# Optimization experiments

Hardware: AMD Instinct MI355X
Metric: run time of the kernel (lower is better)

The kernel has to match this reference:

```python
import jax, jax.numpy as jnp
import numpy as np

GRID_SIZE = 8
SPLINE_ORDER = 3
GRID_LO, GRID_HI = -1.0, 1.0
EPS = 1e-5  # InstanceNorm2d default eps
C = 16
K = GRID_SIZE + SPLINE_ORDER  # number of B-spline basis channels per input channel


def make_grid():
    h = (GRID_HI - GRID_LO) / GRID_SIZE
    # extended knot vector, length grid_size + 2*spline_order + 1
    return jnp.arange(-SPLINE_ORDER, GRID_SIZE + SPLINE_ORDER + 1, dtype=jnp.float32) * h + GRID_LO


def bspline_bases(x, grid):
    # x: [B,C,H,W] -> bases: [B,C,H,W,K] via Cox-de Boor recursion
    xu = x[..., None]
    bases = ((xu >= grid[:-1]) & (xu < grid[1:])).astype(x.dtype)
    for k in range(1, SPLINE_ORDER + 1):
        left = grid[:-(k + 1)]
        right = grid[k:-1]
        delta = jnp.where(right == left, jnp.ones_like(right), right - left)
        bases = ((xu - left) / delta) * bases[..., :-1] + \
                ((grid[k + 1:] - xu) / (grid[k + 1:] - grid[1:-k])) * bases[..., 1:]
    return bases


def conv2d(x, w):
    # NCHW conv, stride 1, padding 1 (kernel 3x3), bias=False as in KANConv2DLayer
    return jax.lax.conv_general_dilated(
        x, w, window_strides=(1, 1), padding=[(1, 1), (1, 1)],
        dimension_numbers=('NCHW', 'OIHW', 'NCHW'))


def instance_norm(x):
    # nn.InstanceNorm2d(affine=False): normalize over H,W per (N,C)
    m = jnp.mean(x, axis=(2, 3), keepdims=True)
    v = jnp.var(x, axis=(2, 3), keepdims=True)
    return (x - m) * jax.lax.rsqrt(v + EPS)


def prelu(x, a):
    return jnp.where(x >= 0, x, a * x)


def kan_conv_layer(x, base_w, spline_w, prelu_a, grid):
    base_out = conv2d(jax.nn.silu(x), base_w)
    b = bspline_bases(x, grid)                      # [B,C,H,W,K]
    B, Cx, H, W, Kx = b.shape
    b = jnp.moveaxis(b, -1, 2).reshape(B, Cx * Kx, H, W)
    spline_out = conv2d(b, spline_w)
    return prelu(instance_norm(base_out + spline_out), prelu_a)


def setup_inputs() -> dict:
    key = jax.random.key(0)
    ks = jax.random.split(key, 5)
    s = 0.05
    return {
        'x': jax.random.normal(ks[0], (4, C, 512, 512), jnp.float32),
        'base_w1': jax.random.normal(ks[1], (C, C, 3, 3), jnp.float32) * s,
        'spline_w1': jax.random.normal(ks[2], (C, C * K, 3, 3), jnp.float32) * s,
        'prelu_a1': jnp.float32(0.25),
        'base_w2': jax.random.normal(ks[3], (C, C, 3, 3), jnp.float32) * s,
        'spline_w2': jax.random.normal(ks[4], (C, C * K, 3, 3), jnp.float32) * s,
        'prelu_a2': jnp.float32(0.25),
    }


def reference(x, base_w1, spline_w1, prelu_a1, base_w2, spline_w2, prelu_a2):
    grid = make_grid()
    y = kan_conv_layer(x, base_w1, spline_w1, prelu_a1, grid)
    y = kan_conv_layer(y, base_w2, spline_w2, prelu_a2, grid)
    return jax.nn.sigmoid(y)
```

## Files before the change

kernel.cpp:

```cpp
#include <hip/hip_runtime.h>
#include <cstddef>
#include <cstdint>

#define HW    512
#define CCH   16
#define HTILE 18
#define NPIX  324
#define NSLOT 12

typedef _Float16 f16x8 __attribute__((ext_vector_type(8)));
typedef float    f32x4 __attribute__((ext_vector_type(4)));

__device__ __forceinline__ float h2f(ushort u) {
    _Float16 h = __builtin_bit_cast(_Float16, u);
    return (float)h;
}
__device__ __forceinline__ ushort f2h(float f) {
    _Float16 h = (_Float16)f;
    return __builtin_bit_cast(ushort, h);
}
__device__ __forceinline__ uint pack2h(float a, float b) {
    return (uint)f2h(a) | ((uint)f2h(b) << 16);
}

__device__ __forceinline__ void derived12(float x, uint* u) {
    float si = x / (1.0f + __expf(-x));
    float t  = fmaf(x, 4.0f, 7.0f);
    t = fminf(fmaxf(t, -1.0f), 15.0f);
    float ft = floorf(t);
    int   ci = (int)ft;
    float uu = t - ft;
    float um = 1.0f - uu;
    float u2 = uu * uu, m2 = um * um;
    float u3 = u2 * uu, m3 = m2 * um;
    const float c16 = 0.16666667f, c23 = 0.66666667f;
    float w0 = u3 * c16;
    float w3 = m3 * c16;
    float w2 = fmaf(0.5f, u3, c23 - u2);
    float w1 = fmaf(0.5f, m3, c23 - m2);
    uint64_t P = (uint64_t)f2h(w3)
               | ((uint64_t)f2h(w2) << 16)
               | ((uint64_t)f2h(w1) << 32)
               | ((uint64_t)f2h(w0) << 48);
    int s = 16 * ci - 48;
    int d = s >> 6;
    int e = s & 63;
    uint64_t Q = P << e;
    uint64_t R = (P >> (63 - e)) >> 1;
    uint64_t O0 = (d == 0) ? Q : (d == -1) ? R : 0ull;
    uint64_t O1 = (d == 1) ? Q : (d ==  0) ? R : 0ull;
    uint64_t O2 = (d == 2) ? Q : (d ==  1) ? R : 0ull;
    O2 = (O2 & 0x0000ffffffffffffull) | ((uint64_t)f2h(si) << 48);
    u[0] = (uint)O0; u[1] = (uint)(O0 >> 32);
    u[2] = (uint)O1; u[3] = (uint)(O1 >> 32);
    u[4] = (uint)O2; u[5] = (uint)(O2 >> 32);
}

__global__ void __launch_bounds__(64) prep_w(
    const float* __restrict__ bw1, const float* __restrict__ sw1,
    const float* __restrict__ bw2, const float* __restrict__ sw2,
    uint4* __restrict__ wtab1, uint4* __restrict__ wtab2,
    float* __restrict__ part1, float* __restrict__ part2)
{
    const int s    = blockIdx.x;
    const int lane = threadIdx.x;
    const float* bw; const float* sw; uint4* wt;
    if (blockIdx.y == 0) { bw = bw1; sw = sw1; wt = wtab1; }
    else                 { bw = bw2; sw = sw2; wt = wtab2; }

    if (s == 0) {
        float* p = (blockIdx.y == 0) ? part1 : part2;
        p[lane] = 0.0f;
        p[64 + lane] = 0.0f;
    }

    const int co = lane & 15, q = lane >> 4;
    const int chunk = s / 27, sl = s - chunk * 27;
    uint u[4];
#pragma unroll
    for (int jj = 0; jj < 4; ++jj) {
        float w[2];
#pragma unroll
        for (int h = 0; h < 2; ++h) {
            int j   = jj * 2 + h;
            int kl  = 32 * sl + 8 * q + j;
            int tap = kl / 96;
            int r   = kl - tap * 96;
            int ci  = r / 12;
            int kv  = r - ci * 12;
            int cin = chunk * 8 + ci;
            w[h] = (kv == 11) ? bw[(co * 16 + cin) * 9 + tap]
                              : sw[(co * 176 + cin * 11 + kv) * 9 + tap];
        }
        u[jj] = pack2h(w[0], w[1]);
    }
    wt[s * 64 + lane] = make_uint4(u[0], u[1], u[2], u[3]);
}

template<bool IN_H, bool OUT_H, bool NORM_IN>
__global__ __launch_bounds__(256, 2) void conv_mfma(
    const void* __restrict__ in_v,
    const uint4* __restrict__ wtab,
    void* __restrict__ out_v,
    const float* __restrict__ stats_in,
    const float* __restrict__ a_in,
    float* __restrict__ part_out)
{
    __shared__ uint4 dt16[NSLOT * NPIX];
    __shared__ float sn[32];

    const int tid  = threadIdx.x;
    const int lane = tid & 63;
    const int wv   = tid >> 6;
    const int m    = lane & 15;
    const int q    = lane >> 4;
    const int bx0  = blockIdx.x * 16;
    const int by0  = blockIdx.y * 16;
    const int b    = blockIdx.z;

    const float*  inf = (const float*)in_v;
    const ushort* inh = (const ushort*)in_v;

    float pa = 0.0f;
    if (NORM_IN) {
        pa = *a_in;
        if (tid < 32) sn[tid] = stats_in[b * 32 + tid];
    }

    f32x4 acc[4];
#pragma unroll
    for (int t = 0; t < 4; ++t) acc[t] = f32x4{0.f, 0.f, 0.f, 0.f};

#pragma unroll 1
    for (int chunk = 0; chunk < 2; ++chunk) {
        __syncthreads();

        float v0[6], v1[6];
        uint  bofs[6], cps[6];
        bool  live[6];
#pragma unroll
        for (int k = 0; k < 6; ++k) {
            int it  = tid + k * 256;
            bool lv = (it < NPIX * 4);
            int cp  = it / NPIX;
            int pix = it - cp * NPIX;
            int py  = pix / 18;
            int px  = pix - py * 18;
            int gy  = by0 + py - 1;
            int gx  = bx0 + px - 1;
            bool ok = lv && ((unsigned)gy < (unsigned)HW)
                         && ((unsigned)gx < (unsigned)HW);
            live[k] = lv;
            cps[k]  = (uint)cp;
            bofs[k] = (uint)(cp * 3 * NPIX + pix);
            float a = -1.0e9f, c = -1.0e9f;
            if (ok) {
                size_t base = ((size_t)(b * CCH + chunk * 8 + cp * 2) << 18)
                            + ((size_t)gy << 9) + gx;
                if (IN_H) { a = h2f(inh[base]); c = h2f(inh[base + (1u << 18)]); }
                else      { a = inf[base];      c = inf[base + (1u << 18)]; }
            }
            v0[k] = a; v1[k] = c;
        }

        uint4 wf[27];
#pragma unroll
        for (int s = 0; s < 27; ++s) wf[s] = wtab[(chunk * 27 + s) * 64 + lane];

#pragma unroll
        for (int k = 0; k < 6; ++k) {
            if (live[k]) {
                float a0 = v0[k], c0 = v1[k];
                if (NORM_IN) {
                    int ci2 = (chunk * 8 + (int)cps[k] * 2) * 2;
                    a0 = (a0 - sn[ci2])     * sn[ci2 + 1];
                    a0 = (a0 >= 0.f) ? a0 : pa * a0;
                    c0 = (c0 - sn[ci2 + 2]) * sn[ci2 + 3];
                    c0 = (c0 >= 0.f) ? c0 : pa * c0;
                }
                uint uA[6], uB[6];
                derived12(a0, uA);
                derived12(c0, uB);
                uint bo = bofs[k];
                dt16[bo]            = make_uint4(uA[0], uA[1], uA[2], uA[3]);
                dt16[bo + NPIX]     = make_uint4(uA[4], uA[5], uB[0], uB[1]);
                dt16[bo + 2 * NPIX] = make_uint4(uB[2], uB[3], uB[4], uB[5]);
            }
        }
        __syncthreads();

        const uint pixbase = (uint)(wv * 72 + m);
#pragma unroll
        for (int j = 0; j < 3; ++j) {
            const uint slotoff = (uint)((j * 4 + q) * NPIX) + pixbase;
#pragma unroll
            for (int tdx = 0; tdx < 3; ++tdx) {
                f16x8 brow[6];
#pragma unroll
                for (int r6 = 0; r6 < 6; ++r6)
                    brow[r6] = *reinterpret_cast<const f16x8*>(
                        &dt16[slotoff + (uint)(r6 * HTILE + tdx)]);
#pragma unroll
                for (int tdy = 0; tdy < 3; ++tdy) {
                    const int s = (tdy * 3 + tdx) * 3 + j;
#pragma unroll
                    for (int t = 0; t < 4; ++t) {
                        acc[t] = __builtin_amdgcn_mfma_f32_16x16x32_f16(
                            __builtin_bit_cast(f16x8, wf[s]), brow[t + tdy],
                            acc[t], 0, 0, 0);
                    }
                }
            }
        }
    }

#pragma unroll
    for (int t = 0; t < 4; ++t) {
        int oy = by0 + wv * 4 + t;
#pragma unroll
        for (int r = 0; r < 4; ++r) {
            int co = q * 4 + r;
            size_t idx = ((size_t)(b * CCH + co) << 18) + ((size_t)oy << 9) + (bx0 + m);
            if (OUT_H) ((ushort*)out_v)[idx] = f2h(acc[t][r]);
            else       ((float*)out_v)[idx]  = acc[t][r];
        }
    }

    float s4[4], q4[4];
#pragma unroll
    for (int r = 0; r < 4; ++r) {
        s4[r] = acc[0][r] + acc[1][r] + acc[2][r] + acc[3][r];
        q4[r] = fmaf(acc[0][r], acc[0][r],
                fmaf(acc[1][r], acc[1][r],
                fmaf(acc[2][r], acc[2][r], acc[3][r] * acc[3][r])));
    }
#pragma unroll
    for (int off = 8; off > 0; off >>= 1) {
#pragma unroll
        for (int r = 0; r < 4; ++r) {
            s4[r] += __shfl_xor(s4[r], off);
            q4[r] += __shfl_xor(q4[r], off);
        }
    }
    __syncthreads();
    float* scr = (float*)dt16;
    if (m == 0) {
#pragma unroll
        for (int r = 0; r < 4; ++r) {
            scr[(wv * 16 + q * 4 + r) * 2 + 0] = s4[r];
            scr[(wv * 16 + q * 4 + r) * 2 + 1] = q4[r];
        }
    }
    __syncthreads();
    if (tid < 32) {
        int co = tid >> 1, which = tid & 1;
        float v = scr[(0 * 16 + co) * 2 + which] + scr[(1 * 16 + co) * 2 + which]
                + scr[(2 * 16 + co) * 2 + which] + scr[(3 * 16 + co) * 2 + which];
        atomicAdd(&part_out[(size_t)(b * CCH + co) * 2 + which], v);
    }
}

__global__ void __launch_bounds__(64) reduce_final(
    const float* __restrict__ part, float* __restrict__ stats)
{
    const int bc = threadIdx.x;
    const float inv = 1.0f / 262144.0f;
    float s  = part[bc * 2];
    float qq = part[bc * 2 + 1];
    float mval = s * inv;
    float var  = qq * inv - mval * mval;
    stats[bc * 2]     = mval;
    stats[bc * 2 + 1] = rsqrtf(var + 1e-5f);
}

__global__ void __launch_bounds__(256) final_sigmoid(
    float* __restrict__ out, const float* __restrict__ stats,
    const float* __restrict__ a_ptr)
{
    const float a = *a_ptr;
    const int i4 = blockIdx.x * 256 + threadIdx.x;
    const int bc = i4 >> 16;
    const float mm = stats[bc * 2];
    const float rr = stats[bc * 2 + 1];
    float4 v = reinterpret_cast<float4*>(out)[i4];
    float t;
    t = (v.x - mm) * rr; t = (t >= 0.f) ? t : a * t; v.x = 1.0f / (1.0f + __expf(-t));
    t = (v.y - mm) * rr; t = (t >= 0.f) ? t : a * t; v.y = 1.0f / (1.0f + __expf(-t));
    t = (v.z - mm) * rr; t = (t >= 0.f) ? t : a * t; v.z = 1.0f / (1.0f + __expf(-t));
    t = (v.w - mm) * rr; t = (t >= 0.f) ? t : a * t; v.w = 1.0f / (1.0f + __expf(-t));
    reinterpret_cast<float4*>(out)[i4] = v;
}

extern "C" void kernel_launch(void* const* d_in, const int* in_sizes, int n_in,
                              void* d_out, int out_size, void* d_ws, size_t ws_size,
                              hipStream_t stream)
{
    const float* x        = (const float*)d_in[0];
    const float* base_w1  = (const float*)d_in[1];
    const float* spline_w1= (const float*)d_in[2];
    const float* prelu_a1 = (const float*)d_in[3];
    const float* base_w2  = (const float*)d_in[4];
    const float* spline_w2= (const float*)d_in[5];
    const float* prelu_a2 = (const float*)d_in[6];
    float* out_f = (float*)d_out;
    char*  wsb   = (char*)d_ws;

    ushort* z1h    = (ushort*)wsb;
    uint4*  wtab1  = (uint4*)(wsb + 33554432);
    uint4*  wtab2  = (uint4*)(wsb + 33609728);
    float*  part1  = (float*)(wsb + 33665024);
    float*  part2  = (float*)(wsb + 33665536);
    float*  stats1 = (float*)(wsb + 33666048);
    float*  stats2 = (float*)(wsb + 33666560);

    dim3 cgrid(HW / 16, HW / 16, 4);
    dim3 cblk(256);

    prep_w<<<dim3(54, 2), 64, 0, stream>>>(base_w1, spline_w1, base_w2, spline_w2,
                                           wtab1, wtab2, part1, part2);

    conv_mfma<false, true, false><<<cgrid, cblk, 0, stream>>>(
        x, wtab1, z1h, nullptr, nullptr, part1);
    reduce_final<<<1, 64, 0, stream>>>(part1, stats1);

    conv_mfma<true, false, true><<<cgrid, cblk, 0, stream>>>(
        z1h, wtab2, out_f, stats1, prelu_a1, part2);
    reduce_final<<<1, 64, 0, stream>>>(part2, stats2);

    final_sigmoid<<<16384, cblk, 0, stream>>>(out_f, stats2, prelu_a2);
}
```

Before: 356.0 us.

## Shrink conv tile to 12 rows, raise occupancy, prefetch next chunk loads

Cuts the output tile from 16x16 to 16x12 rows, which shrinks the LDS staging buffer so three blocks can fit per CU (launch bounds raised to 3). The global loads for the second channel chunk are issued before the first chunk's MFMA loop, so their latency overlaps with compute. Pixel-to-thread mapping is rewritten so each thread loads four channels per pixel. In exchange, halo overhead per output rises (14 staged rows for 12 outputs instead of 18 for 16), the last row of blocks is partial and needs guards, and register pressure under the tighter launch bound may cause spills.

```diff
diff --git a/kernel.cpp b/kernel.cpp
--- a/kernel.cpp
+++ b/kernel.cpp
@@ -4,8 +4,10 @@
 
 #define HW    512
 #define CCH   16
+#define TR    12
 #define HTILE 18
-#define NPIX  324
+#define HTR   14
+#define NPIX2 252
 #define NSLOT 12
 
 typedef _Float16 f16x8 __attribute__((ext_vector_type(8)));
@@ -98,7 +100,7 @@
 }
 
 template<bool IN_H, bool OUT_H, bool NORM_IN>
-__global__ __launch_bounds__(256, 2) void conv_mfma(
+__global__ __launch_bounds__(256, 3) void conv_mfma(
     const void* __restrict__ in_v,
     const uint4* __restrict__ wtab,
     void* __restrict__ out_v,
@@ -106,7 +108,7 @@
     const float* __restrict__ a_in,
     float* __restrict__ part_out)
 {
-    __shared__ uint4 dt16[NSLOT * NPIX];
+    __shared__ uint4 dt16[NSLOT * NPIX2];
     __shared__ float sn[32];
 
     const int tid  = threadIdx.x;
@@ -115,7 +117,7 @@
     const int m    = lane & 15;
     const int q    = lane >> 4;
     const int bx0  = blockIdx.x * 16;
-    const int by0  = blockIdx.y * 16;
+    const int by0  = blockIdx.y * TR;
     const int b    = blockIdx.z;
 
     const float*  inf = (const float*)in_v;
@@ -127,112 +129,142 @@
         if (tid < 32) sn[tid] = stats_in[b * 32 + tid];
     }
 
-    f32x4 acc[4];
-#pragma unroll
-    for (int t = 0; t < 4; ++t) acc[t] = f32x4{0.f, 0.f, 0.f, 0.f};
-
-#pragma unroll 1
-    for (int chunk = 0; chunk < 2; ++chunk) {
-        __syncthreads();
-
-        float v0[6], v1[6];
-        uint  bofs[6], cps[6];
-        bool  live[6];
-#pragma unroll
-        for (int k = 0; k < 6; ++k) {
-            int it  = tid + k * 256;
-            bool lv = (it < NPIX * 4);
-            int cp  = it / NPIX;
-            int pix = it - cp * NPIX;
-            int py  = pix / 18;
-            int px  = pix - py * 18;
-            int gy  = by0 + py - 1;
-            int gx  = bx0 + px - 1;
-            bool ok = lv && ((unsigned)gy < (unsigned)HW)
-                         && ((unsigned)gx < (unsigned)HW);
-            live[k] = lv;
-            cps[k]  = (uint)cp;
-            bofs[k] = (uint)(cp * 3 * NPIX + pix);
-            float a = -1.0e9f, c = -1.0e9f;
-            if (ok) {
-                size_t base = ((size_t)(b * CCH + chunk * 8 + cp * 2) << 18)
-                            + ((size_t)gy << 9) + gx;
-                if (IN_H) { a = h2f(inh[base]); c = h2f(inh[base + (1u << 18)]); }
-                else      { a = inf[base];      c = inf[base + (1u << 18)]; }
+    bool livek[2], okk[2];
+    int  cbk[2];
+    uint yxk[2], bok[2];
+#pragma unroll
+    for (int k = 0; k < 2; ++k) {
+        int it  = tid + k * 256;
+        bool lv = it < 2 * NPIX2;
+        int cpg = (it >= NPIX2) ? 1 : 0;
+        int pix = it - cpg * NPIX2;
+        int py  = pix / HTILE;
+        int px  = pix - py * HTILE;
+        int gy  = by0 + py - 1;
+        int gx  = bx0 + px - 1;
+        livek[k] = lv;
+        okk[k]   = lv && ((unsigned)gy < (unsigned)HW)
+                      && ((unsigned)gx < (unsigned)HW);
+        cbk[k]   = cpg * 4;
+        yxk[k]   = ((uint)gy << 9) + (uint)gx;
+        bok[k]   = (uint)(cpg * 6 * NPIX2 + pix);
+    }
+
+#define STAGE_LOADS(CHUNK, V) do {                                           \
+    _Pragma("unroll")                                                        \
+    for (int k_ = 0; k_ < 2; ++k_) {                                         \
+        _Pragma("unroll")                                                    \
+        for (int c_ = 0; c_ < 4; ++c_) {                                     \
+            float x_ = -1.0e9f;                 \
+            if (okk[k_]) {                                                   \
+                size_t base_ = ((size_t)(b * CCH + (CHUNK) * 8               \
+                               + cbk[k_] + c_) << 18) + yxk[k_];             \
+                if (IN_H) x_ = h2f(inh[base_]);                              \
+                else      x_ = inf[base_];                                   \
+            }                                                                \
+            (V)[k_ * 4 + c_] = x_;                                           \
+        }                                                                    \
+    } } while (0)
+
+#define DERIVE_WRITE(CHUNK, V) do {                                          \
+    _Pragma("unroll")                                                        \
+    for (int k_ = 0; k_ < 2; ++k_) {                                         \
+        if (livek[k_]) {                                                     \
+            _Pragma("unroll")                                                \
+            for (int pr_ = 0; pr_ < 2; ++pr_) {                              \
+                float a0_ = (V)[k_ * 4 + pr_ * 2];                           \
+                float c0_ = (V)[k_ * 4 + pr_ * 2 + 1];                       \
+                if (NORM_IN) {                                               \
+                    int ci2_ = ((CHUNK) * 8 + cbk[k_] + pr_ * 2) * 2;        \
+                    a0_ = (a0_ - sn[ci2_])     * sn[ci2_ + 1];               \
+                    a0_ = (a0_ >= 0.f) ? a0_ : pa * a0_;                     \
+                    c0_ = (c0_ - sn[ci2_ + 2]) * sn[ci2_ + 3];               \
+                    c0_ = (c0_ >= 0.f) ? c0_ : pa * c0_;                     \
+                }                                                            \
+                uint uA_[6], uB_[6];                                         \
+                derived12(a0_, uA_);                                         \
+                derived12(c0_, uB_);                                         \
+                uint bo_ = bok[k_] + (uint)(pr_ * 3 * NPIX2);                \
+                dt16[bo_]             = make_uint4(uA_[0], uA_[1], uA_[2], uA_[3]); \
+                dt16[bo_ + NPIX2]     = make_uint4(uA_[4], uA_[5], uB_[0], uB_[1]); \
+                dt16[bo_ + 2 * NPIX2] = make_uint4(uB_[2], uB_[3], uB_[4], uB_[5]); \
+            }                                                                \
+        }                                                                    \
+    } } while (0)
+
+#define KLOOP(CHUNK) do {                                                    \
+    uint4 wf_[27];                                                           \
+    _Pragma("unroll")                                                        \
+    for (int s_ = 0; s_ < 27; ++s_)                                          \
+        wf_[s_] = wtab[((CHUNK) * 27 + s_) * 64 + lane];                     \
+    const uint pixbase_ = (uint)(wv * 3 * HTILE + m);                        \
+    _Pragma("unroll")                                                        \
+    for (int j_ = 0; j_ < 3; ++j_) {                                         \
+        const uint slotoff_ = (uint)((j_ * 4 + q) * NPIX2) + pixbase_;       \
+        _Pragma("unroll")                                                    \
+        for (int tdx_ = 0; tdx_ < 3; ++tdx_) {                               \
+            f16x8 brow_[5];                                                  \
+            _Pragma("unroll")                                                \
+            for (int r6_ = 0; r6_ < 5; ++r6_)                                \
+                brow_[r6_] = *reinterpret_cast<const f16x8*>(                \
+                    &dt16[slotoff_ + (uint)(r6_ * HTILE + tdx_)]);           \
+            _Pragma("unroll")                                                \
+            for (int tdy_ = 0; tdy_ < 3; ++tdy_) {                           \
+                const int s_ = (tdy_ * 3 + tdx_) * 3 + j_;                   \
+                _Pragma("unroll")                                            \
+                for (int t_ = 0; t_ < 3; ++t_)                               \
+                    acc[t_] = __builtin_amdgcn_mfma_f32_16x16x32_f16(        \
+                        __builtin_bit_cast(f16x8, wf_[s_]),                  \
+                        brow_[t_ + tdy_], acc[t_], 0, 0, 0);                 \
+            }                                                                \
+        }                                                                    \
+    } } while (0)
+
+    f32x4 acc[3];
+#pragma unroll
+    for (int t = 0; t < 3; ++t) acc[t] = f32x4{0.f, 0.f, 0.f, 0.f};
+
+    float va[8], vb[8];
+
+    STAGE_LOADS(0, va);
+    __syncthreads();
+    DERIVE_WRITE(0, va);
+    __syncthreads();
+    STAGE_LOADS(1, vb);
+    KLOOP(0);
+    __syncthreads();
+    DERIVE_WRITE(1, vb);
+    __syncthreads();
+    KLOOP(1);
+
+#pragma unroll
+    for (int t = 0; t < 3; ++t) {
+        int oy = by0 + wv * 3 + t;
+        if (oy < HW) {
+#pragma unroll
+            for (int r = 0; r < 4; ++r) {
+                int co = q * 4 + r;
+                size_t idx = ((size_t)(b * CCH + co) << 18)
+                           + ((size_t)oy << 9) + (bx0 + m);
+                if (OUT_H) ((ushort*)out_v)[idx] = f2h(acc[t][r]);
+                else       ((float*)out_v)[idx]  = acc[t][r];
             }
-            v0[k] = a; v1[k] = c;
-        }
-
-        uint4 wf[27];
-#pragma unroll
-        for (int s = 0; s < 27; ++s) wf[s] = wtab[(chunk * 27 + s) * 64 + lane];
-
-#pragma unroll
-        for (int k = 0; k < 6; ++k) {
-            if (live[k]) {
-                float a0 = v0[k], c0 = v1[k];
-                if (NORM_IN) {
-                    int ci2 = (chunk * 8 + (int)cps[k] * 2) * 2;
-                    a0 = (a0 - sn[ci2])     * sn[ci2 + 1];
-                    a0 = (a0 >= 0.f) ? a0 : pa * a0;
-                    c0 = (c0 - sn[ci2 + 2]) * sn[ci2 + 3];
-                    c0 = (c0 >= 0.f) ? c0 : pa * c0;
-                }
-                uint uA[6], uB[6];
-                derived12(a0, uA);
-                derived12(c0, uB);
-                uint bo = bofs[k];
-                dt16[bo]            = make_uint4(uA[0], uA[1], uA[2], uA[3]);
-                dt16[bo + NPIX]     = make_uint4(uA[4], uA[5], uB[0], uB[1]);
-                dt16[bo + 2 * NPIX] = make_uint4(uB[2], uB[3], uB[4], uB[5]);
+        }
+    }
+
+    float s4[4], q4[4];
+#pragma unroll
+    for (int r = 0; r < 4; ++r) { s4[r] = 0.0f; q4[r] = 0.0f; }
+#pragma unroll
+    for (int t = 0; t < 3; ++t) {
+        int oy = by0 + wv * 3 + t;
+        if (oy < HW) {
+#pragma unroll
+            for (int r = 0; r < 4; ++r) {
+                s4[r] += acc[t][r];
+                q4[r] = fmaf(acc[t][r], acc[t][r], q4[r]);
             }
         }
-        __syncthreads();
-
-        const uint pixbase = (uint)(wv * 72 + m);
-#pragma unroll
-        for (int j = 0; j < 3; ++j) {
-            const uint slotoff = (uint)((j * 4 + q) * NPIX) + pixbase;
-#pragma unroll
-            for (int tdx = 0; tdx < 3; ++tdx) {
-                f16x8 brow[6];
-#pragma unroll
-                for (int r6 = 0; r6 < 6; ++r6)
-                    brow[r6] = *reinterpret_cast<const f16x8*>(
-                        &dt16[slotoff + (uint)(r6 * HTILE + tdx)]);
-#pragma unroll
-                for (int tdy = 0; tdy < 3; ++tdy) {
-                    const int s = (tdy * 3 + tdx) * 3 + j;
-#pragma unroll
-                    for (int t = 0; t < 4; ++t) {
-                        acc[t] = __builtin_amdgcn_mfma_f32_16x16x32_f16(
-                            __builtin_bit_cast(f16x8, wf[s]), brow[t + tdy],
-                            acc[t], 0, 0, 0);
-                    }
-                }
-            }
-        }
-    }
-
-#pragma unroll
-    for (int t = 0; t < 4; ++t) {
-        int oy = by0 + wv * 4 + t;
-#pragma unroll
-        for (int r = 0; r < 4; ++r) {
-            int co = q * 4 + r;
-            size_t idx = ((size_t)(b * CCH + co) << 18) + ((size_t)oy << 9) + (bx0 + m);
-            if (OUT_H) ((ushort*)out_v)[idx] = f2h(acc[t][r]);
-            else       ((float*)out_v)[idx]  = acc[t][r];
-        }
-    }
-
-    float s4[4], q4[4];
-#pragma unroll
-    for (int r = 0; r < 4; ++r) {
-        s4[r] = acc[0][r] + acc[1][r] + acc[2][r] + acc[3][r];
-        q4[r] = fmaf(acc[0][r], acc[0][r],
-                fmaf(acc[1][r], acc[1][r],
-                fmaf(acc[2][r], acc[2][r], acc[3][r] * acc[3][r])));
     }
 #pragma unroll
     for (int off = 8; off > 0; off >>= 1) {
@@ -258,6 +290,9 @@
                 + scr[(2 * 16 + co) * 2 + which] + scr[(3 * 16 + co) * 2 + which];
         atomicAdd(&part_out[(size_t)(b * CCH + co) * 2 + which], v);
     }
+#undef STAGE_LOADS
+#undef DERIVE_WRITE
+#undef KLOOP
 }
 
 __global__ void __launch_bounds__(64) reduce_final(
@@ -313,7 +348,7 @@
     float*  stats1 = (float*)(wsb + 33666048);
     float*  stats2 = (float*)(wsb + 33666560);
 
-    dim3 cgrid(HW / 16, HW / 16, 4);
+    dim3 cgrid(HW / 16, (HW + TR - 1) / TR, 4);
     dim3 cblk(256);
 
     prep_w<<<dim3(54, 2), 64, 0, stream>>>(base_w1, spline_w1, base_w2, spline_w2,
```

After: 415.2 us. 1.17x slower.
